# Kernel optimization log

Hardware: AMD Instinct MI355X
Metric: run time of the kernel (lower is better)

Reference implementation:

```python
import jax, jax.numpy as jnp
import numpy as np

B, I, H = 16384, 512, 512


def setup_inputs() -> dict:
    key = jax.random.key(0)
    ks = jax.random.split(key, 16)
    s_w = 1.0 / np.sqrt(I)  # torch Linear default init scale (uniform bound)
    s_u = 1.0 / np.sqrt(H)
    d = {
        "u": jax.random.normal(ks[0], (B, I), jnp.float32),
        "h": jax.random.normal(ks[1], (B, H), jnp.float32),
        "c": jax.random.normal(ks[2], (B, H), jnp.float32),
        "Wi": jax.random.normal(ks[3], (H, I), jnp.float32) * s_w,
        "bWi": jax.random.normal(ks[4], (H,), jnp.float32) * s_w,
        "Wf": jax.random.normal(ks[5], (H, I), jnp.float32) * s_w,
        "bWf": jax.random.normal(ks[6], (H,), jnp.float32) * s_w,
        "Wg": jax.random.normal(ks[7], (H, I), jnp.float32) * s_w,
        "bWg": jax.random.normal(ks[8], (H,), jnp.float32) * s_w,
        "Wo": jax.random.normal(ks[9], (H, I), jnp.float32) * s_w,
        "bWo": jax.random.normal(ks[10], (H,), jnp.float32) * s_w,
        "Ui": jax.random.normal(ks[11], (H, H), jnp.float32) * s_u,
        "Uf": jax.random.normal(ks[12], (H, H), jnp.float32) * s_u,
        "Ug": jax.random.normal(ks[13], (H, H), jnp.float32) * s_u,
        "Uo": jax.random.normal(ks[14], (H, H), jnp.float32) * s_u,
        "bi": jnp.zeros((H,), jnp.float32),
        "bf": jnp.zeros((H,), jnp.float32),
        "bg": jnp.zeros((H,), jnp.float32),
        "bo": jnp.zeros((H,), jnp.float32),
    }
    return d


def reference(u, h, c, Wi, bWi, Wf, bWf, Wg, bWg, Wo, bWo,
              Ui, Uf, Ug, Uo, bi, bf, bg, bo):
    # Fuse 4 input projections and 4 hidden projections into two GEMMs
    # each producing [B, 4H]; math identical to 8 separate Linears.
    W = jnp.concatenate([Wi, Wf, Wg, Wo], axis=0)        # [4H, I]
    U = jnp.concatenate([Ui, Uf, Ug, Uo], axis=0)        # [4H, H]
    bW = jnp.concatenate([bWi, bWf, bWg, bWo], axis=0)   # Linear biases
    bE = jnp.concatenate([bi, bf, bg, bo], axis=0)       # extra b_* params
    z = u @ W.T + h @ U.T + bW + bE                      # [B, 4H]
    zi, zf, zg, zo = jnp.split(z, 4, axis=-1)
    i = jax.nn.sigmoid(zi)
    f = jax.nn.sigmoid(zf)
    g = jnp.tanh(zg)
    o = jax.nn.sigmoid(zo)
    c_next = f * c + i * g
    h_next = o * jnp.tanh(c_next)
    return (h_next, c_next)
```

## Files before the change

### kernel.cpp

```cpp
#include <hip/hip_runtime.h>
#include <hip/hip_bf16.h>
#include <cstddef>
#include <cstdint>


#define BDIM 16384
#define HDIM 512

typedef __attribute__((ext_vector_type(8))) short bf16x8;
typedef __attribute__((ext_vector_type(4))) float f32x4;

struct Params {
  const float* u;
  const float* h;
  const float* c;
  const float* W[4];
  const float* U[4];
  const float* bW[4];
  const float* bE[4];
  float* outh;
  float* outc;
};

__device__ __forceinline__ float sigmoidf_(float x) {
  return 1.0f / (1.0f + __expf(-x));
}
__device__ __forceinline__ float tanhf_(float x) {
  return 2.0f / (1.0f + __expf(-2.0f * x)) - 1.0f;
}

__device__ __forceinline__ void async16(const void* g, void* l) {
  __builtin_amdgcn_global_load_lds((const __attribute__((address_space(1))) void*)g,
                                   (__attribute__((address_space(3))) void*)l,
                                   16, 0, 0);
}

__device__ __forceinline__ bf16x8 cvt8(f32x4 a, f32x4 b) {
  bf16x8 r;
#pragma unroll
  for (int j = 0; j < 4; ++j) {
    __hip_bfloat16 t = __float2bfloat16(a[j]);
    r[j] = *reinterpret_cast<short*>(&t);
  }
#pragma unroll
  for (int j = 0; j < 4; ++j) {
    __hip_bfloat16 t = __float2bfloat16(b[j]);
    r[4 + j] = *reinterpret_cast<short*>(&t);
  }
  return r;
}

__global__ void cvt_x_kernel(const float* __restrict__ u, const float* __restrict__ h,
                             __hip_bfloat16* __restrict__ Xbf) {
  const size_t e = ((size_t)blockIdx.x * 512 + threadIdx.x) * 8;
  const int r = (int)(e >> 10);
  const int cidx = (int)(e & 1023);
  const float* s = (cidx < 512) ? (u + (size_t)r * 512 + cidx)
                                : (h + (size_t)r * 512 + (cidx - 512));
  f32x4 v0 = *(const f32x4*)s;
  f32x4 v1 = *(const f32x4*)(s + 4);
  *(bf16x8*)(Xbf + e) = cvt8(v0, v1);
}

__global__ void cvt_w_kernel(Params p, __hip_bfloat16* __restrict__ Wbf,
                             float* __restrict__ biasC) {
  const size_t gt = (size_t)blockIdx.x * 512 + threadIdx.x;
  const size_t e = gt * 8;
  const int g = (int)(e >> 19);
  const int rem = (int)(e & 524287);
  const int hcol = rem >> 10;
  const int k = rem & 1023;
  const float* s = (k < 512) ? (p.W[g] + (size_t)hcol * 512 + k)
                             : (p.U[g] + (size_t)hcol * 512 + (k - 512));
  f32x4 v0 = *(const f32x4*)s;
  f32x4 v1 = *(const f32x4*)(s + 4);
  *(bf16x8*)(Wbf + e) = cvt8(v0, v1);
  if (gt < 2048) {
    const int bg = (int)(gt >> 9), hh = (int)(gt & 511);
    biasC[gt] = p.bW[bg][hh] + p.bE[bg][hh];
  }
}

__launch_bounds__(512, 2)
__global__ void lstm_main_kernel(const __hip_bfloat16* __restrict__ Xbf,
                                 const __hip_bfloat16* __restrict__ Wbf,
                                 const float* __restrict__ biasC,
                                 const float* __restrict__ c,
                                 float* __restrict__ outh,
                                 float* __restrict__ outc) {
  __shared__ char smem[131072];

  const int tid = threadIdx.x;
  const int w   = tid >> 6;
  const int l   = tid & 63;
  const int wm  = w >> 2;
  const int wh  = w & 3;

  const int swz = (blockIdx.x & 7) * 64 + (blockIdx.x >> 3);
  const int m_tile = swz & 63;
  const int h_tile = swz >> 6;
  const int rowA0 = m_tile * 256;
  const int nrow0 = h_tile * 64;

  const int rsub = l >> 3;
  const int slot = (l & 7) ^ rsub;
  const int gW = w >> 1;
  const int hrel0 = (w & 1) * 32;

  f32x4 acc[4][8] = {};

  auto stage = [&](int kt, char* bufA, char* bufW) {
    const int kc = kt * 64;
#pragma unroll
    for (int j = 0; j < 4; ++j) {
      const int rit = w * 32 + j * 8 + rsub;
      const __hip_bfloat16* gp = Xbf + (size_t)(rowA0 + rit) * 1024 + kc + slot * 8;
      async16(gp, bufA + (w * 32 + j * 8) * 128);
    }
#pragma unroll
    for (int j = 0; j < 4; ++j) {
      const int hr = hrel0 + j * 8 + rsub;
      const __hip_bfloat16* gp =
          Wbf + (size_t)(gW * 512 + nrow0 + hr) * 1024 + kc + slot * 8;
      async16(gp, bufW + (w * 32 + j * 8) * 128);
    }
  };

  const int xr = (l & 7) << 4;

  auto compute = [&](const char* bufA, const char* bufW) {
#pragma unroll
    for (int kk = 0; kk < 2; ++kk) {
      const int kb = (kk * 64 + (l >> 4) * 16) ^ xr;
      bf16x8 a[8];
#pragma unroll
      for (int mf = 0; mf < 8; ++mf)
        a[mf] = *(const bf16x8*)(bufA + (wm * 128 + mf * 16 + (l & 15)) * 128 + kb);
#pragma unroll
      for (int g = 0; g < 4; ++g) {
        bf16x8 b = *(const bf16x8*)(bufW + (g * 64 + wh * 16 + (l & 15)) * 128 + kb);
#pragma unroll
        for (int mf = 0; mf < 8; ++mf)
          acc[g][mf] = __builtin_amdgcn_mfma_f32_16x16x32_bf16(a[mf], b, acc[g][mf], 0, 0, 0);
      }
    }
  };

  stage(0, smem, smem + 32768);
  __syncthreads();
  int cur = 0;
  for (int kt = 0; kt < 16; ++kt) {
    char* bA = smem + cur * 65536;
    char* nA = smem + (cur ^ 1) * 65536;
    if (kt < 15) stage(kt + 1, nA, nA + 32768);
    compute(bA, bA + 32768);
    __syncthreads();
    cur ^= 1;
  }

  const int lr = (l >> 4) * 4;
  const int lc = l & 15;
  const int hc = nrow0 + wh * 16 + lc;
  const float bzi = biasC[0 * 512 + hc];
  const float bzf = biasC[1 * 512 + hc];
  const float bzg = biasC[2 * 512 + hc];
  const float bzo = biasC[3 * 512 + hc];
#pragma unroll
  for (int mf = 0; mf < 8; ++mf) {
#pragma unroll
    for (int j = 0; j < 4; ++j) {
      const int row = rowA0 + wm * 128 + mf * 16 + lr + j;
      const float zi = acc[0][mf][j] + bzi;
      const float zf = acc[1][mf][j] + bzf;
      const float zg = acc[2][mf][j] + bzg;
      const float zo = acc[3][mf][j] + bzo;
      const float ig = sigmoidf_(zi);
      const float fg = sigmoidf_(zf);
      const float gg = tanhf_(zg);
      const float og = sigmoidf_(zo);
      const size_t idx = (size_t)row * 512 + hc;
      const float cv = c[idx];
      const float cn = fg * cv + ig * gg;
      const float hn = og * tanhf_(cn);
      outh[idx] = hn;
      outc[idx] = cn;
    }
  }
}

__launch_bounds__(256, 2)
__global__ void lstm_legacy_kernel(Params p) {
  __shared__ char smem[32768];
  __shared__ float biasLDS[4][32];

  const int tid = threadIdx.x;
  const int w   = tid >> 6;
  const int l   = tid & 63;
  const int m_tile = blockIdx.x & 127;
  const int h_tile = blockIdx.x >> 7;

  char* smemA = smem;
  char* smemW = smem + 16384;
  const int rowA0 = m_tile * 128;
  const int nrow0 = h_tile * 32;

  if (tid < 128) {
    const int g = tid >> 5, hh = tid & 31;
    const int hc = nrow0 + hh;
    biasLDS[g][hh] = p.bW[g][hc] + p.bE[g][hc];
  }

  const int sr = tid >> 3;
  const int sc = tid & 7;
  const int wcol = (sc * 16) ^ ((sr & 7) << 4);

  f32x4 acc[4][2][2] = {};
  f32x4 rg[16];

  auto load_tile = [&](int kt) {
    const float* sA = (kt < 8) ? p.u : p.h;
    const int kc = (kt & 7) * 64;
#pragma unroll
    for (int cc = 0; cc < 4; ++cc) {
      const float* gp = sA + (size_t)(rowA0 + cc * 32 + sr) * 512 + kc + sc * 8;
      rg[cc * 2]     = *(const f32x4*)gp;
      rg[cc * 2 + 1] = *(const f32x4*)(gp + 4);
    }
#pragma unroll
    for (int cc = 0; cc < 4; ++cc) {
      const float* sW = (kt < 8) ? p.W[cc] : p.U[cc];
      const float* gp = sW + (size_t)(nrow0 + sr) * 512 + kc + sc * 8;
      rg[8 + cc * 2]     = *(const f32x4*)gp;
      rg[8 + cc * 2 + 1] = *(const f32x4*)(gp + 4);
    }
  };

  auto write_tile = [&]() {
#pragma unroll
    for (int cc = 0; cc < 4; ++cc)
      *(bf16x8*)(smemA + (cc * 32 + sr) * 128 + wcol) = cvt8(rg[cc * 2], rg[cc * 2 + 1]);
#pragma unroll
    for (int cc = 0; cc < 4; ++cc)
      *(bf16x8*)(smemW + (cc * 32 + sr) * 128 + wcol) = cvt8(rg[8 + cc * 2], rg[8 + cc * 2 + 1]);
  };

  const int xr = (l & 7) << 4;

  auto compute = [&]() {
#pragma unroll
    for (int kk = 0; kk < 2; ++kk) {
      const int kb = (kk * 64 + (l >> 4) * 16) ^ xr;
      bf16x8 a0 = *(const bf16x8*)(smemA + (w * 32 +      (l & 15)) * 128 + kb);
      bf16x8 a1 = *(const bf16x8*)(smemA + (w * 32 + 16 + (l & 15)) * 128 + kb);
#pragma unroll
      for (int g = 0; g < 4; ++g) {
#pragma unroll
        for (int ni = 0; ni < 2; ++ni) {
          bf16x8 b = *(const bf16x8*)(smemW + (g * 32 + ni * 16 + (l & 15)) * 128 + kb);
          acc[g][0][ni] = __builtin_amdgcn_mfma_f32_16x16x32_bf16(a0, b, acc[g][0][ni], 0, 0, 0);
          acc[g][1][ni] = __builtin_amdgcn_mfma_f32_16x16x32_bf16(a1, b, acc[g][1][ni], 0, 0, 0);
        }
      }
    }
  };

  load_tile(0);
  for (int kt = 0; kt < 16; ++kt) {
    write_tile();
    __syncthreads();
    if (kt < 15) load_tile(kt + 1);
    compute();
    __syncthreads();
  }

  const int lr = (l >> 4) * 4;
  const int lc = l & 15;
#pragma unroll
  for (int mi = 0; mi < 2; ++mi) {
#pragma unroll
    for (int j = 0; j < 4; ++j) {
      const int row = rowA0 + w * 32 + mi * 16 + lr + j;
#pragma unroll
      for (int ni = 0; ni < 2; ++ni) {
        const int hc = nrow0 + ni * 16 + lc;
        const int bcol = ni * 16 + lc;
        const float zi = acc[0][mi][ni][j] + biasLDS[0][bcol];
        const float zf = acc[1][mi][ni][j] + biasLDS[1][bcol];
        const float zg = acc[2][mi][ni][j] + biasLDS[2][bcol];
        const float zo = acc[3][mi][ni][j] + biasLDS[3][bcol];
        const float ig = sigmoidf_(zi);
        const float fg = sigmoidf_(zf);
        const float gg = tanhf_(zg);
        const float og = sigmoidf_(zo);
        const size_t idx = (size_t)row * 512 + hc;
        const float cv = p.c[idx];
        const float cn = fg * cv + ig * gg;
        const float hn = og * tanhf_(cn);
        p.outh[idx] = hn;
        p.outc[idx] = cn;
      }
    }
  }
}

extern "C" void kernel_launch(void* const* d_in, const int* in_sizes, int n_in,
                              void* d_out, int out_size, void* d_ws, size_t ws_size,
                              hipStream_t stream) {
  Params p;
  p.u = (const float*)d_in[0];
  p.h = (const float*)d_in[1];
  p.c = (const float*)d_in[2];
  p.W[0] = (const float*)d_in[3];
  p.bW[0] = (const float*)d_in[4];
  p.W[1] = (const float*)d_in[5];
  p.bW[1] = (const float*)d_in[6];
  p.W[2] = (const float*)d_in[7];
  p.bW[2] = (const float*)d_in[8];
  p.W[3] = (const float*)d_in[9];
  p.bW[3] = (const float*)d_in[10];
  p.U[0] = (const float*)d_in[11];
  p.U[1] = (const float*)d_in[12];
  p.U[2] = (const float*)d_in[13];
  p.U[3] = (const float*)d_in[14];
  p.bE[0] = (const float*)d_in[15];
  p.bE[1] = (const float*)d_in[16];
  p.bE[2] = (const float*)d_in[17];
  p.bE[3] = (const float*)d_in[18];
  p.outh = (float*)d_out;
  p.outc = (float*)d_out + (size_t)BDIM * HDIM;

  const size_t X_BYTES = (size_t)BDIM * 1024 * 2;
  const size_t W_BYTES = (size_t)4 * 512 * 1024 * 2;
  const size_t B_BYTES = 2048 * 4;
  if (ws_size >= X_BYTES + W_BYTES + B_BYTES) {
    __hip_bfloat16* Xbf = (__hip_bfloat16*)d_ws;
    __hip_bfloat16* Wbf = (__hip_bfloat16*)((char*)d_ws + X_BYTES);
    float* biasC = (float*)((char*)d_ws + X_BYTES + W_BYTES);

    hipLaunchKernelGGL(cvt_x_kernel, dim3(4096), dim3(512), 0, stream, p.u, p.h, Xbf);
    hipLaunchKernelGGL(cvt_w_kernel, dim3(512), dim3(512), 0, stream, p, Wbf, biasC);
    hipLaunchKernelGGL(lstm_main_kernel, dim3(512), dim3(512), 0, stream,
                       Xbf, Wbf, biasC, p.c, p.outh, p.outc);
  } else {
    hipLaunchKernelGGL(lstm_legacy_kernel, dim3(2048), dim3(256), 0, stream, p);
  }
}
```

Baseline: 98.95 us.

## Load LSTM weight fragments directly into registers and shrink block tile

The main GEMM kernel now uses 256-thread blocks covering 256 rows by 32 hidden columns (×4 gates), launched as 1024 blocks. Weight fragments are read straight from global memory into registers, double-buffered, instead of being staged through LDS, so shared memory holds only the activation tiles and halves to 64KB. The K loop is unrolled into explicit ping-pong stages. This cuts LDS traffic and footprint and may let more blocks fit per CU. In exchange, the activation tile is reused across half as many columns, so total activation reads from global/L2 roughly double, and register pressure rises.

```diff
diff --git a/kernel.cpp b/kernel.cpp
--- a/kernel.cpp
+++ b/kernel.cpp
@@ -81,81 +81,98 @@
   }
 }
 
-__launch_bounds__(512, 2)
+__launch_bounds__(256, 2)
 __global__ void lstm_main_kernel(const __hip_bfloat16* __restrict__ Xbf,
                                  const __hip_bfloat16* __restrict__ Wbf,
                                  const float* __restrict__ biasC,
                                  const float* __restrict__ c,
                                  float* __restrict__ outh,
                                  float* __restrict__ outc) {
-  __shared__ char smem[131072];
+  __shared__ char smem[65536];
 
   const int tid = threadIdx.x;
   const int w   = tid >> 6;
   const int l   = tid & 63;
-  const int wm  = w >> 2;
-  const int wh  = w & 3;
-
-  const int swz = (blockIdx.x & 7) * 64 + (blockIdx.x >> 3);
+  const int wm  = w >> 1;
+  const int wh  = w & 1;
+
+  const int swz = (blockIdx.x & 7) * 128 + (blockIdx.x >> 3);
   const int m_tile = swz & 63;
   const int h_tile = swz >> 6;
   const int rowA0 = m_tile * 256;
-  const int nrow0 = h_tile * 64;
-
-  const int rsub = l >> 3;
-  const int slot = (l & 7) ^ rsub;
-  const int gW = w >> 1;
-  const int hrel0 = (w & 1) * 32;
+  const int nrow0 = h_tile * 32;
+
+  const int srow = tid >> 3;
+  const int rsub = srow & 7;
+  const int slot = (tid & 7) ^ rsub;
+
+  const __hip_bfloat16* gpA = Xbf + (size_t)(rowA0 + srow) * 1024 + slot * 8;
+  const int dofs = srow * 128 + (tid & 7) * 16;
+
+  const __hip_bfloat16* wp[4];
+#pragma unroll
+  for (int g = 0; g < 4; ++g)
+    wp[g] = Wbf + (size_t)(g * 512 + nrow0 + wh * 16 + (l & 15)) * 1024 + (l >> 4) * 8;
 
   f32x4 acc[4][8] = {};
-
-  auto stage = [&](int kt, char* bufA, char* bufW) {
-    const int kc = kt * 64;
-#pragma unroll
-    for (int j = 0; j < 4; ++j) {
-      const int rit = w * 32 + j * 8 + rsub;
-      const __hip_bfloat16* gp = Xbf + (size_t)(rowA0 + rit) * 1024 + kc + slot * 8;
-      async16(gp, bufA + (w * 32 + j * 8) * 128);
-    }
-#pragma unroll
-    for (int j = 0; j < 4; ++j) {
-      const int hr = hrel0 + j * 8 + rsub;
-      const __hip_bfloat16* gp =
-          Wbf + (size_t)(gW * 512 + nrow0 + hr) * 1024 + kc + slot * 8;
-      async16(gp, bufW + (w * 32 + j * 8) * 128);
-    }
-  };
-
-  const int xr = (l & 7) << 4;
-
-  auto compute = [&](const char* bufA, const char* bufW) {
+  bf16x8 wa[8], wb[8];
+
+  auto STAGE = [&](int t, char* buf) {
+#pragma unroll
+    for (int j = 0; j < 8; ++j)
+      async16(gpA + (size_t)j * 32 * 1024 + t * 64, buf + j * 32 * 128 + dofs);
+  };
+  auto LOADW = [&](int t, bf16x8* wd) {
+#pragma unroll
+    for (int g = 0; g < 4; ++g) {
+      wd[g * 2]     = *(const bf16x8*)(wp[g] + t * 64);
+      wd[g * 2 + 1] = *(const bf16x8*)(wp[g] + t * 64 + 32);
+    }
+  };
+
+  const int xr  = (l & 7) << 4;
+  const int ar  = l & 15;
+  const int kof = (l >> 4) * 16;
+
+  auto COMPUTE = [&](const char* buf, const bf16x8* wd) {
 #pragma unroll
     for (int kk = 0; kk < 2; ++kk) {
-      const int kb = (kk * 64 + (l >> 4) * 16) ^ xr;
-      bf16x8 a[8];
-#pragma unroll
-      for (int mf = 0; mf < 8; ++mf)
-        a[mf] = *(const bf16x8*)(bufA + (wm * 128 + mf * 16 + (l & 15)) * 128 + kb);
-#pragma unroll
-      for (int g = 0; g < 4; ++g) {
-        bf16x8 b = *(const bf16x8*)(bufW + (g * 64 + wh * 16 + (l & 15)) * 128 + kb);
-#pragma unroll
-        for (int mf = 0; mf < 8; ++mf)
-          acc[g][mf] = __builtin_amdgcn_mfma_f32_16x16x32_bf16(a[mf], b, acc[g][mf], 0, 0, 0);
+      const int kb = (kk * 64 + kof) ^ xr;
+#pragma unroll
+      for (int mh = 0; mh < 2; ++mh) {
+        bf16x8 av[4];
+#pragma unroll
+        for (int i = 0; i < 4; ++i)
+          av[i] = *(const bf16x8*)(buf + (wm * 128 + (mh * 4 + i) * 16 + ar) * 128 + kb);
+#pragma unroll
+        for (int g = 0; g < 4; ++g)
+#pragma unroll
+          for (int i = 0; i < 4; ++i)
+            acc[g][mh * 4 + i] = __builtin_amdgcn_mfma_f32_16x16x32_bf16(
+                av[i], wd[g * 2 + kk], acc[g][mh * 4 + i], 0, 0, 0);
       }
     }
   };
 
-  stage(0, smem, smem + 32768);
+  char* buf0 = smem;
+  char* buf1 = smem + 32768;
+
+  STAGE(0, buf0);
+  LOADW(0, wa);
   __syncthreads();
-  int cur = 0;
-  for (int kt = 0; kt < 16; ++kt) {
-    char* bA = smem + cur * 65536;
-    char* nA = smem + (cur ^ 1) * 65536;
-    if (kt < 15) stage(kt + 1, nA, nA + 32768);
-    compute(bA, bA + 32768);
+
+  for (int tt = 0; tt < 8; ++tt) {
+    const int t = tt * 2;
+    STAGE(t + 1, buf1);
+    LOADW(t + 1, wb);
+    COMPUTE(buf0, wa);
     __syncthreads();
-    cur ^= 1;
+    if (t + 2 < 16) {
+      STAGE(t + 2, buf0);
+      LOADW(t + 2, wa);
+    }
+    COMPUTE(buf1, wb);
+    __syncthreads();
   }
 
   const int lr = (l >> 4) * 4;
@@ -206,8 +223,8 @@
 
   if (tid < 128) {
     const int g = tid >> 5, hh = tid & 31;
-    const int hc = nrow0 + hh;
-    biasLDS[g][hh] = p.bW[g][hc] + p.bE[g][hc];
+    const int hcb = nrow0 + hh;
+    biasLDS[g][hh] = p.bW[g][hcb] + p.bE[g][hcb];
   }
 
   const int sr = tid >> 3;
@@ -282,7 +299,7 @@
       const int row = rowA0 + w * 32 + mi * 16 + lr + j;
 #pragma unroll
       for (int ni = 0; ni < 2; ++ni) {
-        const int hc = nrow0 + ni * 16 + lc;
+        const int hcc = nrow0 + ni * 16 + lc;
         const int bcol = ni * 16 + lc;
         const float zi = acc[0][mi][ni][j] + biasLDS[0][bcol];
         const float zf = acc[1][mi][ni][j] + biasLDS[1][bcol];
@@ -292,7 +309,7 @@
         const float fg = sigmoidf_(zf);
         const float gg = tanhf_(zg);
         const float og = sigmoidf_(zo);
-        const size_t idx = (size_t)row * 512 + hc;
+        const size_t idx = (size_t)row * 512 + hcc;
         const float cv = p.c[idx];
         const float cn = fg * cv + ig * gg;
         const float hn = og * tanhf_(cn);
@@ -339,7 +356,7 @@
 
     hipLaunchKernelGGL(cvt_x_kernel, dim3(4096), dim3(512), 0, stream, p.u, p.h, Xbf);
     hipLaunchKernelGGL(cvt_w_kernel, dim3(512), dim3(512), 0, stream, p, Wbf, biasC);
-    hipLaunchKernelGGL(lstm_main_kernel, dim3(512), dim3(512), 0, stream,
+    hipLaunchKernelGGL(lstm_main_kernel, dim3(1024), dim3(256), 0, stream,
                        Xbf, Wbf, biasC, p.c, p.outh, p.outc);
   } else {
     hipLaunchKernelGGL(lstm_legacy_kernel, dim3(2048), dim3(256), 0, stream, p);
```

After: 146.1 us. +47.7%, slower.

## Split GEMM main loop into fine-grained staged load/compute phases with explicit waitcnts

Applied to the files above, without the earlier changes.

Replaces the simple double-buffered stage/compute loop with a four-phase schedule per K tile. Each phase issues part of the next tiles' async global-to-LDS copies, reads a quarter of the fragments, and runs MFMAs under raised wave priority. Explicit vmcnt/lgkmcnt waits, sched barriers and raw s_barriers replace __syncthreads, aiming to overlap memory traffic with MFMA work in a ping-pong style. The cost is more barriers and fragile hand-tuned wait counts that could race or stall if the counts are wrong.

```diff
diff --git a/kernel.cpp b/kernel.cpp
--- a/kernel.cpp
+++ b/kernel.cpp
@@ -81,6 +81,18 @@
   }
 }
 
+#define VM6 asm volatile("s_waitcnt vmcnt(6)" ::: "memory")
+#define VM0 asm volatile("s_waitcnt vmcnt(0)" ::: "memory")
+#define LG0 asm volatile("s_waitcnt lgkmcnt(0)" ::: "memory")
+#define LG8 asm volatile("s_waitcnt lgkmcnt(8)" ::: "memory")
+#define FENCE __builtin_amdgcn_sched_barrier(0)
+#define BAR                                  \
+  do {                                       \
+    asm volatile("" ::: "memory");           \
+    __builtin_amdgcn_s_barrier();            \
+    asm volatile("" ::: "memory");           \
+  } while (0)
+
 __launch_bounds__(512, 2)
 __global__ void lstm_main_kernel(const __hip_bfloat16* __restrict__ Xbf,
                                  const __hip_bfloat16* __restrict__ Wbf,
@@ -102,60 +114,101 @@
   const int rowA0 = m_tile * 256;
   const int nrow0 = h_tile * 64;
 
-  const int rsub = l >> 3;
-  const int slot = (l & 7) ^ rsub;
-  const int gW = w >> 1;
-  const int hrel0 = (w & 1) * 32;
+  const int trow = tid >> 3;
+  const int rsub = trow & 7;
+  const int slot8 = ((tid & 7) ^ rsub) * 8;
+  const int dofs = trow * 128 + (tid & 7) * 16;
+
+  const __hip_bfloat16* srcA = Xbf + (size_t)(rowA0 + trow) * 1024 + slot8;
+  const __hip_bfloat16* srcW = Wbf + (size_t)(nrow0 + trow) * 1024 + slot8;
 
   f32x4 acc[4][8] = {};
 
-  auto stage = [&](int kt, char* bufA, char* bufW) {
-    const int kc = kt * 64;
-#pragma unroll
-    for (int j = 0; j < 4; ++j) {
-      const int rit = w * 32 + j * 8 + rsub;
-      const __hip_bfloat16* gp = Xbf + (size_t)(rowA0 + rit) * 1024 + kc + slot * 8;
-      async16(gp, bufA + (w * 32 + j * 8) * 128);
-    }
-#pragma unroll
-    for (int j = 0; j < 4; ++j) {
-      const int hr = hrel0 + j * 8 + rsub;
-      const __hip_bfloat16* gp =
-          Wbf + (size_t)(gW * 512 + nrow0 + hr) * 1024 + kc + slot * 8;
-      async16(gp, bufW + (w * 32 + j * 8) * 128);
-    }
-  };
-
-  const int xr = (l & 7) << 4;
-
-  auto compute = [&](const char* bufA, const char* bufW) {
-#pragma unroll
-    for (int kk = 0; kk < 2; ++kk) {
-      const int kb = (kk * 64 + (l >> 4) * 16) ^ xr;
-      bf16x8 a[8];
-#pragma unroll
-      for (int mf = 0; mf < 8; ++mf)
-        a[mf] = *(const bf16x8*)(bufA + (wm * 128 + mf * 16 + (l & 15)) * 128 + kb);
-#pragma unroll
-      for (int g = 0; g < 4; ++g) {
-        bf16x8 b = *(const bf16x8*)(bufW + (g * 64 + wh * 16 + (l & 15)) * 128 + kb);
-#pragma unroll
-        for (int mf = 0; mf < 8; ++mf)
-          acc[g][mf] = __builtin_amdgcn_mfma_f32_16x16x32_bf16(a[mf], b, acc[g][mf], 0, 0, 0);
-      }
-    }
-  };
-
-  stage(0, smem, smem + 32768);
-  __syncthreads();
-  int cur = 0;
-  for (int kt = 0; kt < 16; ++kt) {
-    char* bA = smem + cur * 65536;
-    char* nA = smem + (cur ^ 1) * 65536;
-    if (kt < 15) stage(kt + 1, nA, nA + 32768);
-    compute(bA, bA + 32768);
-    __syncthreads();
-    cur ^= 1;
+  const int xr  = (l & 7) << 4;
+  const int ar  = l & 15;
+  const int kb0 = ((l >> 4) * 16) ^ xr;
+  const int kb1 = (64 + (l >> 4) * 16) ^ xr;
+
+  auto ST_A = [&](int t, int h) {
+    char* d = smem + ((t & 1) << 16) + h * 64 * 128 + dofs;
+    const __hip_bfloat16* s = srcA + (size_t)(h * 64) * 1024 + t * 64;
+    async16(s, d);
+    async16(s + (size_t)128 * 1024, d + 128 * 128);
+  };
+  auto ST_B = [&](int t, int G) {
+    char* d = smem + ((t & 1) << 16) + 32768 + G * 128 * 128 + dofs;
+    const __hip_bfloat16* s = srcW + (size_t)(G * 2 * 512) * 1024 + t * 64;
+    async16(s, d);
+    async16(s + (size_t)512 * 1024, d + 64 * 128);
+  };
+  auto RD_A = [&](const char* sA, int mh, bf16x8* d) {
+#pragma unroll
+    for (int mf = 0; mf < 4; ++mf) {
+      const char* p = sA + (wm * 128 + mh * 64 + mf * 16 + ar) * 128;
+      d[mf * 2 + 0] = *(const bf16x8*)(p + kb0);
+      d[mf * 2 + 1] = *(const bf16x8*)(p + kb1);
+    }
+  };
+  auto RD_B = [&](const char* sB, int G, bf16x8* d) {
+#pragma unroll
+    for (int g2 = 0; g2 < 2; ++g2) {
+      const char* p = sB + ((G * 2 + g2) * 64 + wh * 16 + ar) * 128;
+      d[g2 * 2 + 0] = *(const bf16x8*)(p + kb0);
+      d[g2 * 2 + 1] = *(const bf16x8*)(p + kb1);
+    }
+  };
+  auto MM = [&](int mh, int G, const bf16x8* a, const bf16x8* b) {
+    __builtin_amdgcn_s_setprio(1);
+#pragma unroll
+    for (int g2 = 0; g2 < 2; ++g2)
+#pragma unroll
+      for (int mf = 0; mf < 4; ++mf)
+#pragma unroll
+        for (int kk = 0; kk < 2; ++kk)
+          acc[G * 2 + g2][mh * 4 + mf] = __builtin_amdgcn_mfma_f32_16x16x32_bf16(
+              a[mf * 2 + kk], b[g2 * 2 + kk], acc[G * 2 + g2][mh * 4 + mf], 0, 0, 0);
+    __builtin_amdgcn_s_setprio(0);
+  };
+
+  ST_A(0, 0); ST_B(0, 0); ST_B(0, 1); ST_A(0, 1);
+  ST_A(1, 0); ST_B(1, 0); ST_B(1, 1);
+  VM6; FENCE;
+  BAR;
+
+  bf16x8 aF[8], b0[4], b1[4];
+
+  for (int t = 0; t < 16; ++t) {
+    const char* sA = smem + ((t & 1) << 16);
+    const char* sB = sA + 32768;
+
+    RD_A(sA, 0, aF);
+    RD_B(sB, 0, b0);
+    if (t + 1 < 16) ST_A(t + 1, 1);
+    LG8;
+    BAR;
+    LG0; FENCE;
+    MM(0, 0, aF, b0);
+    BAR;
+
+    RD_B(sB, 1, b1);
+    if (t + 2 < 16) ST_A(t + 2, 0);
+    BAR;
+    LG0; FENCE;
+    MM(0, 1, aF, b1);
+    BAR;
+
+    RD_A(sA, 1, aF);
+    if (t + 2 < 16) ST_B(t + 2, 0);
+    BAR;
+    LG0; FENCE;
+    MM(1, 0, aF, b0);
+    BAR;
+
+    if (t + 2 < 16) ST_B(t + 2, 1);
+    MM(1, 1, aF, b1);
+    if (t == 14) { VM0; } else { VM6; }
+    FENCE;
+    BAR;
   }
 
   const int lr = (l >> 4) * 4;
@@ -206,8 +259,8 @@
 
   if (tid < 128) {
     const int g = tid >> 5, hh = tid & 31;
-    const int hc = nrow0 + hh;
-    biasLDS[g][hh] = p.bW[g][hc] + p.bE[g][hc];
+    const int hcb = nrow0 + hh;
+    biasLDS[g][hh] = p.bW[g][hcb] + p.bE[g][hcb];
   }
 
   const int sr = tid >> 3;
@@ -282,7 +335,7 @@
       const int row = rowA0 + w * 32 + mi * 16 + lr + j;
 #pragma unroll
       for (int ni = 0; ni < 2; ++ni) {
-        const int hc = nrow0 + ni * 16 + lc;
+        const int hcc = nrow0 + ni * 16 + lc;
         const int bcol = ni * 16 + lc;
         const float zi = acc[0][mi][ni][j] + biasLDS[0][bcol];
         const float zf = acc[1][mi][ni][j] + biasLDS[1][bcol];
@@ -292,7 +345,7 @@
         const float fg = sigmoidf_(zf);
         const float gg = tanhf_(zg);
         const float og = sigmoidf_(zo);
-        const size_t idx = (size_t)row * 512 + hc;
+        const size_t idx = (size_t)row * 512 + hcc;
         const float cv = p.c[idx];
         const float cn = fg * cv + ig * gg;
         const float hn = og * tanhf_(cn);
```

Result: slower. 108.0 us (+9.1%).
